# Optimization experiments

Measured on AMD Instinct MI355X. Metric: run time of the kernel, lower is better.

Reference implementation:

```python
import jax, jax.numpy as jnp
import numpy as np
from jax import lax

D_MODEL = 512
EXPAND = 2
INNER = D_MODEL * EXPAND
K = 4
B, T = 8, 2048
LN_EPS = 1e-5


def setup_inputs() -> dict:
    key = jax.random.key(0)
    ks = jax.random.split(key, 12)
    s_in = 1.0 / np.sqrt(D_MODEL)
    s_out = 1.0 / np.sqrt(INNER)
    return {
        "x": jax.random.normal(ks[0], (B, T, D_MODEL), dtype=jnp.float32),
        "ln_w": jnp.ones((D_MODEL,), jnp.float32),
        "ln_b": jnp.zeros((D_MODEL,), jnp.float32),
        "in_proj_w": jax.random.uniform(ks[1], (3 * INNER, D_MODEL), jnp.float32, -s_in, s_in),
        "in_proj_b": jax.random.uniform(ks[2], (3 * INNER,), jnp.float32, -s_in, s_in),
        "conv_w": jax.random.uniform(ks[3], (INNER, 1, K), jnp.float32, -0.5, 0.5),
        "conv_b": jax.random.uniform(ks[4], (INNER,), jnp.float32, -0.5, 0.5),
        "delta_w": jax.random.uniform(ks[5], (INNER, D_MODEL), jnp.float32, -s_in, s_in),
        "delta_b": jax.random.uniform(ks[6], (INNER,), jnp.float32, -s_in, s_in),
        "state_mix": jnp.zeros((INNER,), jnp.float32),
        "skip_scale": jnp.ones((INNER,), jnp.float32),
        "out_proj_w": jax.random.uniform(ks[7], (D_MODEL, INNER), jnp.float32, -s_out, s_out),
        "out_proj_b": jax.random.uniform(ks[8], (D_MODEL,), jnp.float32, -s_out, s_out),
    }


def _layernorm(x, w, b):
    mu = jnp.mean(x, axis=-1, keepdims=True)
    var = jnp.mean(jnp.square(x - mu), axis=-1, keepdims=True)
    return (x - mu) * lax.rsqrt(var + LN_EPS) * w + b


def _causal_dw_conv(x_bct, w, b):
    # x: [B, C, T], w: [C, 1, K] depthwise, left pad K-1 (causal)
    y = lax.conv_general_dilated(
        x_bct, w, window_strides=(1,), padding=[(K - 1, 0)],
        dimension_numbers=("NCH", "OIH", "NCH"), feature_group_count=INNER)
    return y + b[None, :, None]


def reference(x, ln_w, ln_b, in_proj_w, in_proj_b, conv_w, conv_b,
              delta_w, delta_b, state_mix, skip_scale, out_proj_w, out_proj_b):
    residual = x
    xn = _layernorm(x, ln_w, ln_b)                      # [B,T,D]
    h = xn @ in_proj_w.T + in_proj_b                     # [B,T,3*INNER]
    proj, gate, drive = jnp.split(h, 3, axis=-1)
    proj = jax.nn.silu(proj)
    gate = jax.nn.sigmoid(gate)
    conv_out = _causal_dw_conv(jnp.swapaxes(proj, 1, 2), conv_w, conv_b)
    conv_out = jnp.swapaxes(conv_out, 1, 2)              # [B,T,INNER]
    delta = jnp.maximum(jax.nn.sigmoid(xn @ delta_w.T + delta_b), 1e-4)
    drive = jnp.tanh(drive)
    a = jax.nn.sigmoid(state_mix)                        # [INNER]
    d = delta * drive                                    # [B,T,INNER]

    def step(state, d_t):
        state = a * state + d_t
        return state, state

    _, states = lax.scan(step, jnp.zeros((x.shape[0], INNER), x.dtype),
                         jnp.swapaxes(d, 0, 1))          # [T,B,INNER]
    states = jnp.swapaxes(states, 0, 1)                  # [B,T,INNER]
    y = (states + skip_scale * conv_out) * gate
    y = y @ out_proj_w.T + out_proj_b
    return residual + y
```

## Files before the change

### kernel.cpp

```cpp
#include <hip/hip_runtime.h>
#include <stdint.h>

#define D_MODEL 512
#define INNER   1024
#define NCAT    4096
#define BATCH   8
#define SEQ     2048
#define ROWS    (BATCH*SEQ)
#define LN_EPS  1e-5f
#define CHUNK   64
#define NCHUNK  (SEQ/CHUNK)

typedef unsigned short u16;
typedef unsigned int   u32;
typedef __attribute__((ext_vector_type(8))) short bf16x8;
typedef __attribute__((ext_vector_type(4))) float f32x4;

__device__ __forceinline__ u16 f2bf(float f) {
  u32 u = __builtin_bit_cast(u32, f);
  return (u16)((u + 0x7FFFu + ((u >> 16) & 1u)) >> 16);
}
__device__ __forceinline__ float bf2f(u32 lo) {
  return __builtin_bit_cast(float, lo << 16);
}
__device__ __forceinline__ float sigf(float x){ return 1.f/(1.f+__expf(-x)); }

__device__ __forceinline__ void glds16(const void* g, void* l) {
  __builtin_amdgcn_global_load_lds((const __attribute__((address_space(1))) void*)g,
                                   (__attribute__((address_space(3))) void*)l, 16, 0, 0);
}

#define MFMA16(a,b,c) __builtin_amdgcn_mfma_f32_16x16x32_bf16((a),(b),(c),0,0,0)

__global__ __launch_bounds__(256) void ln_kernel(const float* __restrict__ x,
    const float* __restrict__ lw, const float* __restrict__ lb,
    u16* __restrict__ xn) {
  const int row  = blockIdx.x * 4 + (threadIdx.x >> 6);
  const int lane = threadIdx.x & 63;
  const float4* xr = (const float4*)(x + (size_t)row * D_MODEL);
  float4 v0 = xr[lane*2], v1 = xr[lane*2+1];
  float s  = v0.x+v0.y+v0.z+v0.w + v1.x+v1.y+v1.z+v1.w;
  float s2 = v0.x*v0.x+v0.y*v0.y+v0.z*v0.z+v0.w*v0.w
           + v1.x*v1.x+v1.y*v1.y+v1.z*v1.z+v1.w*v1.w;
  #pragma unroll
  for (int o=32;o;o>>=1){ s += __shfl_xor(s,o); s2 += __shfl_xor(s2,o); }
  const float mu = s * (1.f/D_MODEL);
  const float rs = rsqrtf(s2*(1.f/D_MODEL) - mu*mu + LN_EPS);
  const float4* wv = (const float4*)lw; const float4* bv = (const float4*)lb;
  float4 w0 = wv[lane*2], w1 = wv[lane*2+1];
  float4 b0 = bv[lane*2], b1 = bv[lane*2+1];
  u32 p0 = (u32)f2bf((v0.x-mu)*rs*w0.x+b0.x) | ((u32)f2bf((v0.y-mu)*rs*w0.y+b0.y)<<16);
  u32 p1 = (u32)f2bf((v0.z-mu)*rs*w0.z+b0.z) | ((u32)f2bf((v0.w-mu)*rs*w0.w+b0.w)<<16);
  u32 p2 = (u32)f2bf((v1.x-mu)*rs*w1.x+b1.x) | ((u32)f2bf((v1.y-mu)*rs*w1.y+b1.y)<<16);
  u32 p3 = (u32)f2bf((v1.z-mu)*rs*w1.z+b1.z) | ((u32)f2bf((v1.w-mu)*rs*w1.w+b1.w)<<16);
  ((uint4*)(xn + (size_t)row * D_MODEL))[lane] = make_uint4(p0,p1,p2,p3);
}

__global__ __launch_bounds__(256) void cvt_all_kernel(const float* __restrict__ ipw,
    const float* __restrict__ dw, const float* __restrict__ opw,
    const float* __restrict__ ipb, const float* __restrict__ db,
    u16* __restrict__ wcat, u16* __restrict__ wout, float* __restrict__ bcat) {
  const int i = blockIdx.x*256 + threadIdx.x;
  const int NW1 = NCAT*D_MODEL, NW2 = D_MODEL*INNER, STR = gridDim.x*256;
  for (int idx = i; idx < NW1; idx += STR) {
    const int r = idx >> 9, c = idx & 511;
    float v;
    if (r < 2048) v = ipw[idx];
    else {
      const int rr = r - 2048;
      v = (rr & 1) ? dw[(size_t)(rr>>1)*D_MODEL + c]
                   : ipw[(size_t)(2048 + (rr>>1))*D_MODEL + c];
    }
    wcat[idx] = f2bf(v);
  }
  for (int idx = i; idx < NW2; idx += STR) wout[idx] = f2bf(opw[idx]);
  if (i < NCAT) {
    float b;
    if (i < 2048) b = ipb[i];
    else { const int rr = i - 2048; b = (rr & 1) ? db[rr>>1] : ipb[2048 + (rr>>1)]; }
    bcat[i] = b;
  }
}

__device__ __forceinline__ void sched_blk(int nbm, int nbn, int GM, int GN,
                                          int& bM, int& bN) {
  const int nwg = nbm * nbn;
  const int bid = blockIdx.x;
  const int cpx = nwg >> 3;
  const int swz = (bid & 7) * cpx + (bid >> 3);
  const int gsz = GM * GN;
  const int g   = swz / gsz, loc = swz - g * gsz;
  const int ngn = nbn / GN;
  const int gm  = g / ngn,  gn  = g - gm * ngn;
  bM = gm * GM + (loc % GM);
  bN = gn * GN + (loc / GM);
}

__device__ __forceinline__ void gemm_main(const u16* __restrict__ A,
    const u16* __restrict__ Bm, int K, int nkt, int bM, int bN,
    u16* lA, u16* lB, f32x4 acc[4][4]) {
  const int tid = threadIdx.x;
  const int l6  = tid >> 2;
  const int sg  = (tid & 3) ^ (l6 & 3);
  const int pB  = (l6 & 15) * 4 + ((l6 >> 4) & 3);
  const u16* gA = A  + (size_t)(bM*128 + l6)*K + sg*8;
  const u16* gB = Bm + (size_t)(bN*128 + pB)*K + sg*8;
  u16* dA = lA + tid*8;
  u16* dB = lB + tid*8;
  const size_t rstep = (size_t)64*K;

#define STAGE_T(koff, bufo) do { \
    const u16* sA = gA + (koff); const u16* sB = gB + (koff); \
    glds16(sA,         dA + (bufo));        glds16(sA + rstep, dA + (bufo) + 2048); \
    glds16(sB,         dB + (bufo));        glds16(sB + rstep, dB + (bufo) + 2048); \
  } while (0)

  STAGE_T(0, 0);
  STAGE_T(32, 4096);
  asm volatile("s_waitcnt vmcnt(4)" ::: "memory");
  __builtin_amdgcn_s_barrier();
  __builtin_amdgcn_sched_barrier(0);

  const int lane = tid & 63, wv = tid >> 6;
  const int wm = wv >> 1, wn = wv & 1;
  const int kx = ((lane>>4) ^ (lane&3)) * 8;
  const int aoff = (wm*64 + (lane&15))*32 + kx;
  const int boff = (wn*64 + (lane&15))*32 + kx;

  int cur = 0, stg = 8192;
  for (int kt = 0; kt < nkt; ++kt) {
    bf16x8 af[4], bfr[4];
    #pragma unroll
    for (int m=0;m<4;m++) af[m]  = *(const bf16x8*)&lA[cur + aoff + m*512];
    #pragma unroll
    for (int n=0;n<4;n++) bfr[n] = *(const bf16x8*)&lB[cur + boff + n*512];
    if (kt + 2 < nkt) STAGE_T((kt+2)*32, stg);
    #pragma unroll
    for (int m=0;m<4;m++)
      #pragma unroll
      for (int n=0;n<4;n++)
        acc[m][n] = MFMA16(af[m], bfr[n], acc[m][n]);
    if (kt + 2 < nkt) { asm volatile("s_waitcnt vmcnt(4)" ::: "memory"); }
    else              { asm volatile("s_waitcnt vmcnt(0)" ::: "memory"); }
    __builtin_amdgcn_s_barrier();
    __builtin_amdgcn_sched_barrier(0);
    cur += 4096; if (cur == 12288) cur = 0;
    stg += 4096; if (stg == 12288) stg = 0;
  }
#undef STAGE_T
}

__global__ __launch_bounds__(256, 3) void gemm1_kernel(const u16* __restrict__ A,
    const u16* __restrict__ Bm, const float* __restrict__ bcat,
    u16* __restrict__ proj, u16* __restrict__ gate, u16* __restrict__ dbuf) {
  __shared__ u16 lA[12288], lB[12288];
  f32x4 acc[4][4];
  #pragma unroll
  for (int m=0;m<4;m++)
    #pragma unroll
    for (int n=0;n<4;n++) acc[m][n] = (f32x4){0.f,0.f,0.f,0.f};
  int bM, bN; sched_blk(ROWS/128, NCAT/128, 16, 8, bM, bN);
  gemm_main(A, Bm, D_MODEL, D_MODEL/32, bM, bN, lA, lB, acc);
  const int lane = threadIdx.x & 63, wv = threadIdx.x >> 6;
  const int wm = wv>>1, wn = wv&1;
  const int colb = bN*128 + wn*64 + (lane&15)*4;
  const float4 b4 = *(const float4*)&bcat[colb];
  const float* bp = (const float*)&b4;
  if (colb < 2048) {
    u16* outp = (colb < 1024) ? proj : gate;
    const int lcolb = colb & (INNER-1);
    #pragma unroll
    for (int m=0;m<4;m++) {
      const int row0 = bM*128 + wm*64 + m*16 + ((lane>>4)<<2);
      #pragma unroll
      for (int r=0;r<4;r++) {
        float a4[4];
        #pragma unroll
        for (int n=0;n<4;n++) {
          float v = acc[m][n][r] + bp[n];
          a4[n] = (colb < 1024) ? v * sigf(v) : sigf(v);
        }
        u32 lo = (u32)f2bf(a4[0]) | ((u32)f2bf(a4[1])<<16);
        u32 hi = (u32)f2bf(a4[2]) | ((u32)f2bf(a4[3])<<16);
        *(uint2*)&outp[(size_t)(row0+r)*INNER + lcolb] = make_uint2(lo, hi);
      }
    }
  } else {
    const int ch0 = (colb - 2048) >> 1;
    #pragma unroll
    for (int m=0;m<4;m++) {
      const int row0 = bM*128 + wm*64 + m*16 + ((lane>>4)<<2);
      #pragma unroll
      for (int r=0;r<4;r++) {
        const float v0 = acc[m][0][r] + bp[0];
        const float v1 = acc[m][1][r] + bp[1];
        const float v2 = acc[m][2][r] + bp[2];
        const float v3 = acc[m][3][r] + bp[3];
        const float d0 = (2.f*sigf(2.f*v0) - 1.f) * fmaxf(sigf(v1), 1e-4f);
        const float d1 = (2.f*sigf(2.f*v2) - 1.f) * fmaxf(sigf(v3), 1e-4f);
        *(u32*)&dbuf[(size_t)(row0+r)*INNER + ch0] = (u32)f2bf(d0) | ((u32)f2bf(d1)<<16);
      }
    }
  }
}

__global__ __launch_bounds__(256, 3) void gemm2_kernel(const u16* __restrict__ A,
    const u16* __restrict__ Bm, const float* __restrict__ ob,
    const float* __restrict__ resid, float* __restrict__ out) {
  __shared__ u16 lA[12288], lB[12288];
  f32x4 acc[4][4];
  #pragma unroll
  for (int m=0;m<4;m++)
    #pragma unroll
    for (int n=0;n<4;n++) acc[m][n] = (f32x4){0.f,0.f,0.f,0.f};
  int bM, bN; sched_blk(ROWS/128, D_MODEL/128, 8, 4, bM, bN);
  gemm_main(A, Bm, INNER, INNER/32, bM, bN, lA, lB, acc);
  const int lane = threadIdx.x & 63, wv = threadIdx.x >> 6;
  const int wm = wv>>1, wn = wv&1;
  const int colb = bN*128 + wn*64 + (lane&15)*4;
  const float4 ob4 = *(const float4*)&ob[colb];
  #pragma unroll
  for (int m=0;m<4;m++) {
    const int row0 = bM*128 + wm*64 + m*16 + ((lane>>4)<<2);
    #pragma unroll
    for (int r=0;r<4;r++) {
      const size_t idx = (size_t)(row0+r)*D_MODEL + colb;
      float4 rs = *(const float4*)&resid[idx];
      float4 o;
      o.x = acc[m][0][r] + ob4.x + rs.x;
      o.y = acc[m][1][r] + ob4.y + rs.y;
      o.z = acc[m][2][r] + ob4.z + rs.z;
      o.w = acc[m][3][r] + ob4.w + rs.w;
      *(float4*)&out[idx] = o;
    }
  }
}

__global__ __launch_bounds__(256) void scan1_kernel(const u16* __restrict__ d,
    const float* __restrict__ sm, float* __restrict__ cS) {
  const int blk = blockIdx.x;
  const int half = blk & 1, ch = (blk>>1) & (NCHUNK-1), b = blk >> 6;
  const int c0 = half*512 + threadIdx.x*2;
  const float a0 = sigf(sm[c0]), a1 = sigf(sm[c0+1]);
  float s0 = 0.f, s1 = 0.f;
  size_t base = ((size_t)b*SEQ + ch*CHUNK)*INNER + c0;
  for (int t=0;t<CHUNK;t++) {
    u32 du = *(const u32*)(d + base);
    s0 = a0*s0 + bf2f(du & 0xffffu);
    s1 = a1*s1 + bf2f(du >> 16);
    base += INNER;
  }
  const size_t o = ((size_t)b*NCHUNK + ch)*INNER + c0;
  cS[o] = s0; cS[o+1] = s1;
}

__global__ __launch_bounds__(256) void scan2_kernel(const float* __restrict__ sm,
    const float* __restrict__ cS, float* __restrict__ carry) {
  const int idx = blockIdx.x*256 + threadIdx.x;
  const int b = idx >> 9, c0 = (idx & 511)*2;
  const float a0 = sigf(sm[c0]), a1 = sigf(sm[c0+1]);
  float A0 = a0, A1 = a1;
  #pragma unroll
  for (int i=0;i<6;i++){ A0*=A0; A1*=A1; }
  float cr0 = 0.f, cr1 = 0.f;
  for (int ch=0; ch<NCHUNK; ch++) {
    const size_t o = ((size_t)b*NCHUNK + ch)*INNER + c0;
    carry[o] = cr0; carry[o+1] = cr1;
    cr0 = A0*cr0 + cS[o];
    cr1 = A1*cr1 + cS[o+1];
  }
}

__global__ __launch_bounds__(256) void scan3_kernel(const u16* __restrict__ proj,
    const u16* __restrict__ gate, const u16* __restrict__ d,
    const float* __restrict__ carry, const float* __restrict__ sm,
    const float* __restrict__ cw, const float* __restrict__ cb,
    const float* __restrict__ sk, u16* __restrict__ z) {
  const int blk = blockIdx.x;
  const int half = blk & 1, ch = (blk>>1) & (NCHUNK-1), b = blk >> 6;
  const int c0 = half*512 + threadIdx.x*2;
  const float a0 = sigf(sm[c0]), a1 = sigf(sm[c0+1]);
  const float cb0 = cb[c0], cb1 = cb[c0+1];
  const float sk0 = sk[c0], sk1 = sk[c0+1];
  const float w00=cw[c0*4+0], w01=cw[c0*4+1], w02=cw[c0*4+2], w03=cw[c0*4+3];
  const float w10=cw[c0*4+4], w11=cw[c0*4+5], w12=cw[c0*4+6], w13=cw[c0*4+7];
  const size_t o = ((size_t)b*NCHUNK + ch)*INNER + c0;
  float s0 = carry[o], s1 = carry[o+1];
  const int t0 = ch*CHUNK;
  const size_t rowb = (size_t)b*SEQ*INNER + c0;
  float pa0=0,pb0=0,pc0=0, pa1=0,pb1=0,pc1=0;
  if (ch > 0) {
    u32 u3 = *(const u32*)(proj + rowb + (size_t)(t0-3)*INNER);
    u32 u2 = *(const u32*)(proj + rowb + (size_t)(t0-2)*INNER);
    u32 u1 = *(const u32*)(proj + rowb + (size_t)(t0-1)*INNER);
    pa0 = bf2f(u3&0xffffu); pa1 = bf2f(u3>>16);
    pb0 = bf2f(u2&0xffffu); pb1 = bf2f(u2>>16);
    pc0 = bf2f(u1&0xffffu); pc1 = bf2f(u1>>16);
  }
  size_t base = rowb + (size_t)t0*INNER;
  for (int t=0;t<CHUNK;t++) {
    u32 pu = *(const u32*)(proj + base);
    const float pd0 = bf2f(pu&0xffffu), pd1 = bf2f(pu>>16);
    const float co0 = w00*pa0 + w01*pb0 + w02*pc0 + w03*pd0 + cb0;
    const float co1 = w10*pa1 + w11*pb1 + w12*pc1 + w13*pd1 + cb1;
    pa0=pb0; pb0=pc0; pc0=pd0;  pa1=pb1; pb1=pc1; pc1=pd1;
    u32 du = *(const u32*)(d + base);
    s0 = a0*s0 + bf2f(du&0xffffu);
    s1 = a1*s1 + bf2f(du>>16);
    u32 gu = *(const u32*)(gate + base);
    const float z0 = (s0 + sk0*co0)*bf2f(gu&0xffffu);
    const float z1 = (s1 + sk1*co1)*bf2f(gu>>16);
    *(u32*)(z + base) = (u32)f2bf(z0) | ((u32)f2bf(z1)<<16);
    base += INNER;
  }
}

extern "C" void kernel_launch(void* const* d_in, const int* in_sizes, int n_in,
                              void* d_out, int out_size, void* d_ws, size_t ws_size,
                              hipStream_t stream) {
  const float* x    = (const float*)d_in[0];
  const float* ln_w = (const float*)d_in[1];
  const float* ln_b = (const float*)d_in[2];
  const float* ipw  = (const float*)d_in[3];
  const float* ipb  = (const float*)d_in[4];
  const float* cw   = (const float*)d_in[5];
  const float* cb   = (const float*)d_in[6];
  const float* dw   = (const float*)d_in[7];
  const float* db   = (const float*)d_in[8];
  const float* sm   = (const float*)d_in[9];
  const float* sk   = (const float*)d_in[10];
  const float* opw  = (const float*)d_in[11];
  const float* opb  = (const float*)d_in[12];
  float* out = (float*)d_out;

  uint8_t* w = (uint8_t*)d_ws;
  u16* xn    = (u16*)w;  w += (size_t)ROWS*D_MODEL*2;
  u16* wcat  = (u16*)w;  w += (size_t)NCAT*D_MODEL*2;
  u16* wout  = (u16*)w;  w += (size_t)D_MODEL*INNER*2;
  u16* proj  = (u16*)w;  w += (size_t)ROWS*INNER*2;
  u16* gate  = (u16*)w;  w += (size_t)ROWS*INNER*2;
  u16* dbuf  = (u16*)w;  w += (size_t)ROWS*INNER*2;
  u16* z     = (u16*)w;  w += (size_t)ROWS*INNER*2;
  float* cS    = (float*)w; w += (size_t)BATCH*NCHUNK*INNER*4;
  float* carry = (float*)w; w += (size_t)BATCH*NCHUNK*INNER*4;
  float* bcat  = (float*)w; w += (size_t)NCAT*4;

  ln_kernel<<<ROWS/4, 256, 0, stream>>>(x, ln_w, ln_b, xn);
  cvt_all_kernel<<<1024, 256, 0, stream>>>(ipw, dw, opw, ipb, db, wcat, wout, bcat);
  gemm1_kernel<<<(ROWS/128)*(NCAT/128), 256, 0, stream>>>(xn, wcat, bcat, proj, gate, dbuf);
  scan1_kernel<<<BATCH*NCHUNK*2, 256, 0, stream>>>(dbuf, sm, cS);
  scan2_kernel<<<16, 256, 0, stream>>>(sm, cS, carry);
  scan3_kernel<<<BATCH*NCHUNK*2, 256, 0, stream>>>(proj, gate, dbuf, carry, sm, cw, cb, sk, z);
  gemm2_kernel<<<(ROWS/128)*(D_MODEL/128), 256, 0, stream>>>(z, wout, opb, x, out);
}
```

Measured before the change: 168.1 us.

## Enlarge gemm1 to 256x256 tiles with 512 threads and dynamic LDS

Rewrites the first projection GEMM as a standalone kernel using 256x256 output tiles, 8 waves each computing 128x64, with a new swizzled LDS layout held in 96KB of dynamic shared memory across three stages. The larger tile raises arithmetic intensity and cuts global and LDS traffic per FLOP for the dominant GEMM. In exchange, occupancy drops to at most 2 blocks per CU, register pressure rises with 32 accumulators per thread, and the grid shrinks to 1024 blocks, which may leave wave-quantisation tail effects.

```diff
diff --git a/kernel.cpp b/kernel.cpp
--- a/kernel.cpp
+++ b/kernel.cpp
@@ -96,82 +96,83 @@
   bN = gn * GN + (loc / GM);
 }
 
-__device__ __forceinline__ void gemm_main(const u16* __restrict__ A,
-    const u16* __restrict__ Bm, int K, int nkt, int bM, int bN,
-    u16* lA, u16* lB, f32x4 acc[4][4]) {
+__global__ __launch_bounds__(512, 2) void gemm1_kernel(const u16* __restrict__ A,
+    const u16* __restrict__ Bm, const float* __restrict__ bcat,
+    u16* __restrict__ proj, u16* __restrict__ gate, u16* __restrict__ dbuf) {
+  extern __shared__ u16 lds[];
   const int tid = threadIdx.x;
-  const int l6  = tid >> 2;
-  const int sg  = (tid & 3) ^ (l6 & 3);
-  const int pB  = (l6 & 15) * 4 + ((l6 >> 4) & 3);
-  const u16* gA = A  + (size_t)(bM*128 + l6)*K + sg*8;
-  const u16* gB = Bm + (size_t)(bN*128 + pB)*K + sg*8;
-  u16* dA = lA + tid*8;
-  u16* dB = lB + tid*8;
-  const size_t rstep = (size_t)64*K;
-
-#define STAGE_T(koff, bufo) do { \
-    const u16* sA = gA + (koff); const u16* sB = gB + (koff); \
-    glds16(sA,         dA + (bufo));        glds16(sA + rstep, dA + (bufo) + 2048); \
-    glds16(sB,         dB + (bufo));        glds16(sB + rstep, dB + (bufo) + 2048); \
-  } while (0)
-
-  STAGE_T(0, 0);
-  STAGE_T(32, 4096);
+  int bM, bN; sched_blk(ROWS/256, NCAT/256, 8, 4, bM, bN);
+
+  const u16* gA0; const u16* gA1; const u16* gB0; const u16* gB1;
+  {
+    const int p0 = tid,        q0 = p0>>3, t0 = (p0&7) ^ (q0&7);
+    const int p1 = 512 + tid,  q1 = p1>>3, t1 = (p1&7) ^ (q1&7);
+    const int rA0 = q0*2 + (t0>>2), sA0 = t0&3;
+    const int rA1 = q1*2 + (t1>>2), sA1 = t1&3;
+    gA0 = A + (size_t)(bM*256 + rA0)*D_MODEL + sA0*8;
+    gA1 = A + (size_t)(bM*256 + rA1)*D_MODEL + sA1*8;
+    const int c0 = (rA0 & ~63) + ((rA0&15)*4) + ((rA0>>4)&3);
+    const int c1 = (rA1 & ~63) + ((rA1&15)*4) + ((rA1>>4)&3);
+    gB0 = Bm + (size_t)(bN*256 + c0)*D_MODEL + sA0*8;
+    gB1 = Bm + (size_t)(bN*256 + c1)*D_MODEL + sA1*8;
+  }
+
+#define STAGE1(KOFF, BUFO) do { \
+    glds16(gA0 + (KOFF), lds + (BUFO) + tid*8); \
+    glds16(gA1 + (KOFF), lds + (BUFO) + 4096 + tid*8); \
+    glds16(gB0 + (KOFF), lds + (BUFO) + 8192 + tid*8); \
+    glds16(gB1 + (KOFF), lds + (BUFO) + 12288 + tid*8); } while(0)
+
+  const int lane = tid & 63, wid = tid >> 6;
+  const int wm = wid >> 2, wn = wid & 3;
+  const int rl = lane & 15;
+  const int e  = (((lane&1)<<2) + (lane>>4)) ^ (rl>>1);
+  const int aoff = wm*4096 + (rl>>1)*64 + e*8;
+  const int boff = 8192 + wn*2048 + (rl>>1)*64 + e*8;
+
+  f32x4 acc[8][4];
+  #pragma unroll
+  for (int m=0;m<8;m++)
+    #pragma unroll
+    for (int n=0;n<4;n++) acc[m][n] = (f32x4){0.f,0.f,0.f,0.f};
+
+  STAGE1(0, 0);
+  STAGE1(32, 16384);
   asm volatile("s_waitcnt vmcnt(4)" ::: "memory");
   __builtin_amdgcn_s_barrier();
   __builtin_amdgcn_sched_barrier(0);
 
-  const int lane = tid & 63, wv = tid >> 6;
-  const int wm = wv >> 1, wn = wv & 1;
-  const int kx = ((lane>>4) ^ (lane&3)) * 8;
-  const int aoff = (wm*64 + (lane&15))*32 + kx;
-  const int boff = (wn*64 + (lane&15))*32 + kx;
-
-  int cur = 0, stg = 8192;
-  for (int kt = 0; kt < nkt; ++kt) {
-    bf16x8 af[4], bfr[4];
-    #pragma unroll
-    for (int m=0;m<4;m++) af[m]  = *(const bf16x8*)&lA[cur + aoff + m*512];
-    #pragma unroll
-    for (int n=0;n<4;n++) bfr[n] = *(const bf16x8*)&lB[cur + boff + n*512];
-    if (kt + 2 < nkt) STAGE_T((kt+2)*32, stg);
-    #pragma unroll
-    for (int m=0;m<4;m++)
+  int cur = 0, stg = 32768;
+  for (int kt = 0; kt < 16; ++kt) {
+    bf16x8 af[8], bfr[4];
+    #pragma unroll
+    for (int m=0;m<8;m++) af[m]  = *(const bf16x8*)&lds[cur + aoff + m*512];
+    #pragma unroll
+    for (int n=0;n<4;n++) bfr[n] = *(const bf16x8*)&lds[cur + boff + n*512];
+    if (kt + 2 < 16) STAGE1((kt+2)*32, stg);
+    #pragma unroll
+    for (int m=0;m<8;m++)
       #pragma unroll
       for (int n=0;n<4;n++)
         acc[m][n] = MFMA16(af[m], bfr[n], acc[m][n]);
-    if (kt + 2 < nkt) { asm volatile("s_waitcnt vmcnt(4)" ::: "memory"); }
-    else              { asm volatile("s_waitcnt vmcnt(0)" ::: "memory"); }
+    if (kt + 2 < 16) { asm volatile("s_waitcnt vmcnt(4)" ::: "memory"); }
+    else             { asm volatile("s_waitcnt vmcnt(0)" ::: "memory"); }
     __builtin_amdgcn_s_barrier();
     __builtin_amdgcn_sched_barrier(0);
-    cur += 4096; if (cur == 12288) cur = 0;
-    stg += 4096; if (stg == 12288) stg = 0;
-  }
-#undef STAGE_T
-}
-
-__global__ __launch_bounds__(256, 3) void gemm1_kernel(const u16* __restrict__ A,
-    const u16* __restrict__ Bm, const float* __restrict__ bcat,
-    u16* __restrict__ proj, u16* __restrict__ gate, u16* __restrict__ dbuf) {
-  __shared__ u16 lA[12288], lB[12288];
-  f32x4 acc[4][4];
-  #pragma unroll
-  for (int m=0;m<4;m++)
-    #pragma unroll
-    for (int n=0;n<4;n++) acc[m][n] = (f32x4){0.f,0.f,0.f,0.f};
-  int bM, bN; sched_blk(ROWS/128, NCAT/128, 16, 8, bM, bN);
-  gemm_main(A, Bm, D_MODEL, D_MODEL/32, bM, bN, lA, lB, acc);
-  const int lane = threadIdx.x & 63, wv = threadIdx.x >> 6;
-  const int wm = wv>>1, wn = wv&1;
-  const int colb = bN*128 + wn*64 + (lane&15)*4;
+    cur += 16384; if (cur == 49152) cur = 0;
+    stg += 16384; if (stg == 49152) stg = 0;
+  }
+#undef STAGE1
+
+  const int colb = bN*256 + wn*64 + rl*4;
   const float4 b4 = *(const float4*)&bcat[colb];
   const float* bp = (const float*)&b4;
   if (colb < 2048) {
     u16* outp = (colb < 1024) ? proj : gate;
     const int lcolb = colb & (INNER-1);
     #pragma unroll
-    for (int m=0;m<4;m++) {
-      const int row0 = bM*128 + wm*64 + m*16 + ((lane>>4)<<2);
+    for (int m=0;m<8;m++) {
+      const int row0 = bM*256 + wm*128 + m*16 + ((lane>>4)<<2);
       #pragma unroll
       for (int r=0;r<4;r++) {
         float a4[4];
@@ -188,8 +189,8 @@
   } else {
     const int ch0 = (colb - 2048) >> 1;
     #pragma unroll
-    for (int m=0;m<4;m++) {
-      const int row0 = bM*128 + wm*64 + m*16 + ((lane>>4)<<2);
+    for (int m=0;m<8;m++) {
+      const int row0 = bM*256 + wm*128 + m*16 + ((lane>>4)<<2);
       #pragma unroll
       for (int r=0;r<4;r++) {
         const float v0 = acc[m][0][r] + bp[0];
@@ -202,6 +203,60 @@
       }
     }
   }
+}
+
+__device__ __forceinline__ void gemm_main(const u16* __restrict__ A,
+    const u16* __restrict__ Bm, int K, int nkt, int bM, int bN,
+    u16* lA, u16* lB, f32x4 acc[4][4]) {
+  const int tid = threadIdx.x;
+  const int l6  = tid >> 2;
+  const int sg  = (tid & 3) ^ (l6 & 3);
+  const int pB  = (l6 & 15) * 4 + ((l6 >> 4) & 3);
+  const u16* gA = A  + (size_t)(bM*128 + l6)*K + sg*8;
+  const u16* gB = Bm + (size_t)(bN*128 + pB)*K + sg*8;
+  u16* dA = lA + tid*8;
+  u16* dB = lB + tid*8;
+  const size_t rstep = (size_t)64*K;
+
+#define STAGE_T(koff, bufo) do { \
+    const u16* sA = gA + (koff); const u16* sB = gB + (koff); \
+    glds16(sA,         dA + (bufo));        glds16(sA + rstep, dA + (bufo) + 2048); \
+    glds16(sB,         dB + (bufo));        glds16(sB + rstep, dB + (bufo) + 2048); \
+  } while (0)
+
+  STAGE_T(0, 0);
+  STAGE_T(32, 4096);
+  asm volatile("s_waitcnt vmcnt(4)" ::: "memory");
+  __builtin_amdgcn_s_barrier();
+  __builtin_amdgcn_sched_barrier(0);
+
+  const int lane = tid & 63, wv = tid >> 6;
+  const int wm = wv >> 1, wn = wv & 1;
+  const int kx = ((lane>>4) ^ (lane&3)) * 8;
+  const int aoff = (wm*64 + (lane&15))*32 + kx;
+  const int boff = (wn*64 + (lane&15))*32 + kx;
+
+  int cur = 0, stg = 8192;
+  for (int kt = 0; kt < nkt; ++kt) {
+    bf16x8 af[4], bfr[4];
+    #pragma unroll
+    for (int m=0;m<4;m++) af[m]  = *(const bf16x8*)&lA[cur + aoff + m*512];
+    #pragma unroll
+    for (int n=0;n<4;n++) bfr[n] = *(const bf16x8*)&lB[cur + boff + n*512];
+    if (kt + 2 < nkt) STAGE_T((kt+2)*32, stg);
+    #pragma unroll
+    for (int m=0;m<4;m++)
+      #pragma unroll
+      for (int n=0;n<4;n++)
+        acc[m][n] = MFMA16(af[m], bfr[n], acc[m][n]);
+    if (kt + 2 < nkt) { asm volatile("s_waitcnt vmcnt(4)" ::: "memory"); }
+    else              { asm volatile("s_waitcnt vmcnt(0)" ::: "memory"); }
+    __builtin_amdgcn_s_barrier();
+    __builtin_amdgcn_sched_barrier(0);
+    cur += 4096; if (cur == 12288) cur = 0;
+    stg += 4096; if (stg == 12288) stg = 0;
+  }
+#undef STAGE_T
 }
 
 __global__ __launch_bounds__(256, 3) void gemm2_kernel(const u16* __restrict__ A,
@@ -347,7 +402,7 @@
 
   ln_kernel<<<ROWS/4, 256, 0, stream>>>(x, ln_w, ln_b, xn);
   cvt_all_kernel<<<1024, 256, 0, stream>>>(ipw, dw, opw, ipb, db, wcat, wout, bcat);
-  gemm1_kernel<<<(ROWS/128)*(NCAT/128), 256, 0, stream>>>(xn, wcat, bcat, proj, gate, dbuf);
+  gemm1_kernel<<<(ROWS/256)*(NCAT/256), 512, 98304, stream>>>(xn, wcat, bcat, proj, gate, dbuf);
   scan1_kernel<<<BATCH*NCHUNK*2, 256, 0, stream>>>(dbuf, sm, cS);
   scan2_kernel<<<16, 256, 0, stream>>>(sm, cS, carry);
   scan3_kernel<<<BATCH*NCHUNK*2, 256, 0, stream>>>(proj, gate, dbuf, carry, sm, cw, cb, sk, z);
```

New measurement: 173.8 us. 3.4% more time.

## Rewrite gemm1 as 256x256 tile, 8-wave ping-pong pipelined kernel

Applied to the files above, without the earlier changes.

Replaces the 128x128 tile, 4-wave gemm1 with a 256x256 tile, 512-thread kernel that uses 128KB of dynamic LDS with K=64 double buffering. Loads are split into half-tiles interleaved with four MFMA phases, and s_setprio plus barriers coordinate waves. The larger tile raises arithmetic intensity and cuts global traffic. The phased schedule tries to overlap global-to-LDS copies with MFMA work. In exchange, occupancy drops and register pressure rises, since each wave holds 32 accumulators, and the launch needs 128KB of shared memory per block.

```diff
diff --git a/kernel.cpp b/kernel.cpp
--- a/kernel.cpp
+++ b/kernel.cpp
@@ -96,82 +96,127 @@
   bN = gn * GN + (loc / GM);
 }
 
-__device__ __forceinline__ void gemm_main(const u16* __restrict__ A,
-    const u16* __restrict__ Bm, int K, int nkt, int bM, int bN,
-    u16* lA, u16* lB, f32x4 acc[4][4]) {
+__global__ __launch_bounds__(512, 2) void gemm1_kernel(const u16* __restrict__ A,
+    const u16* __restrict__ Bm, const float* __restrict__ bcat,
+    u16* __restrict__ proj, u16* __restrict__ gate, u16* __restrict__ dbuf) {
+  extern __shared__ u16 lds[];
   const int tid = threadIdx.x;
-  const int l6  = tid >> 2;
-  const int sg  = (tid & 3) ^ (l6 & 3);
-  const int pB  = (l6 & 15) * 4 + ((l6 >> 4) & 3);
-  const u16* gA = A  + (size_t)(bM*128 + l6)*K + sg*8;
-  const u16* gB = Bm + (size_t)(bN*128 + pB)*K + sg*8;
-  u16* dA = lA + tid*8;
-  u16* dB = lB + tid*8;
-  const size_t rstep = (size_t)64*K;
-
-#define STAGE_T(koff, bufo) do { \
-    const u16* sA = gA + (koff); const u16* sB = gB + (koff); \
-    glds16(sA,         dA + (bufo));        glds16(sA + rstep, dA + (bufo) + 2048); \
-    glds16(sB,         dB + (bufo));        glds16(sB + rstep, dB + (bufo) + 2048); \
-  } while (0)
-
-  STAGE_T(0, 0);
-  STAGE_T(32, 4096);
+  int bM, bN; sched_blk(ROWS/256, NCAT/256, 8, 4, bM, bN);
+
+  const int rS = tid >> 3;
+  const int cS = (tid & 7) ^ (rS & 7);
+  const u16* gAb = A  + (size_t)(bM*256 + rS)*D_MODEL + cS*8;
+  const u16* gBb = Bm + (size_t)(bN*256 + (rS&15)*4 + ((rS>>4)&3))*D_MODEL + cS*8;
+
+#define SA(h, kt, slot) do { \
+    glds16(gAb + (size_t)(h)*65536 + (kt)*64,         lds + (slot) + (h)*8192 + tid*8); \
+    glds16(gAb + (size_t)(h)*65536 + 32768 + (kt)*64, lds + (slot) + (h)*8192 + 4096 + tid*8); } while(0)
+#define SB(h, kt, slot) do { \
+    glds16(gBb + (size_t)(h)*65536 + (kt)*64,         lds + (slot) + 16384 + (h)*8192 + tid*8); \
+    glds16(gBb + (size_t)(h)*65536 + 32768 + (kt)*64, lds + (slot) + 16384 + (h)*8192 + 4096 + tid*8); } while(0)
+
+  const int lane = tid & 63, wid = tid >> 6;
+  const int wm = wid >> 2, wn = wid & 3;
+  const int ksw = ((lane>>4) ^ (lane&7)) * 8;
+  const int aW = wm*8192 + (lane&15)*64 + ksw;
+  const int bW = 16384 + wn*4096 + (lane&15)*64 + ksw;
+
+  f32x4 acc[8][4];
+  #pragma unroll
+  for (int m=0;m<8;m++)
+    #pragma unroll
+    for (int n=0;n<4;n++) acc[m][n] = (f32x4){0.f,0.f,0.f,0.f};
+  bf16x8 af[4][2], bf0[2][2], bf1[2][2];
+
+#define RD_A(mh, s) do { _Pragma("unroll") \
+    for (int mm=0; mm<4; ++mm) { \
+      af[mm][0] = *(const bf16x8*)&lds[(s) + aW + (mh)*4096 + mm*1024]; \
+      af[mm][1] = *(const bf16x8*)&lds[((s) + aW + (mh)*4096 + mm*1024) ^ 32]; \
+    } } while(0)
+#define RD_B0(s) do { \
+    bf0[0][0] = *(const bf16x8*)&lds[(s) + bW];            bf0[0][1] = *(const bf16x8*)&lds[((s) + bW) ^ 32]; \
+    bf0[1][0] = *(const bf16x8*)&lds[(s) + bW + 1024];     bf0[1][1] = *(const bf16x8*)&lds[((s) + bW + 1024) ^ 32]; } while(0)
+#define RD_B1(s) do { \
+    bf1[0][0] = *(const bf16x8*)&lds[(s) + bW + 2048];     bf1[0][1] = *(const bf16x8*)&lds[((s) + bW + 2048) ^ 32]; \
+    bf1[1][0] = *(const bf16x8*)&lds[(s) + bW + 3072];     bf1[1][1] = *(const bf16x8*)&lds[((s) + bW + 3072) ^ 32]; } while(0)
+#define PH_SYNC do { \
+    __builtin_amdgcn_s_barrier(); \
+    asm volatile("s_waitcnt lgkmcnt(0)" ::: "memory"); \
+    __builtin_amdgcn_sched_barrier(0); \
+    __builtin_amdgcn_s_setprio(1); } while(0)
+#define PH_END do { \
+    __builtin_amdgcn_s_setprio(0); \
+    __builtin_amdgcn_s_barrier(); } while(0)
+#define MM_Q(ML, NL, BF) do { _Pragma("unroll") \
+    for (int mm=0; mm<4; ++mm) { \
+      acc[(ML)+mm][(NL)  ] = MFMA16(af[mm][0], BF[0][0], acc[(ML)+mm][(NL)  ]); \
+      acc[(ML)+mm][(NL)  ] = MFMA16(af[mm][1], BF[0][1], acc[(ML)+mm][(NL)  ]); \
+      acc[(ML)+mm][(NL)+1] = MFMA16(af[mm][0], BF[1][0], acc[(ML)+mm][(NL)+1]); \
+      acc[(ML)+mm][(NL)+1] = MFMA16(af[mm][1], BF[1][1], acc[(ML)+mm][(NL)+1]); \
+    } } while(0)
+
+  SA(0,0,0); SA(1,0,0); SB(0,0,0); SB(1,0,0);
+  SB(0,1,32768); SB(1,1,32768);
   asm volatile("s_waitcnt vmcnt(4)" ::: "memory");
   __builtin_amdgcn_s_barrier();
-  __builtin_amdgcn_sched_barrier(0);
-
-  const int lane = tid & 63, wv = tid >> 6;
-  const int wm = wv >> 1, wn = wv & 1;
-  const int kx = ((lane>>4) ^ (lane&3)) * 8;
-  const int aoff = (wm*64 + (lane&15))*32 + kx;
-  const int boff = (wn*64 + (lane&15))*32 + kx;
-
-  int cur = 0, stg = 8192;
-  for (int kt = 0; kt < nkt; ++kt) {
-    bf16x8 af[4], bfr[4];
-    #pragma unroll
-    for (int m=0;m<4;m++) af[m]  = *(const bf16x8*)&lA[cur + aoff + m*512];
-    #pragma unroll
-    for (int n=0;n<4;n++) bfr[n] = *(const bf16x8*)&lB[cur + boff + n*512];
-    if (kt + 2 < nkt) STAGE_T((kt+2)*32, stg);
-    #pragma unroll
-    for (int m=0;m<4;m++)
-      #pragma unroll
-      for (int n=0;n<4;n++)
-        acc[m][n] = MFMA16(af[m], bfr[n], acc[m][n]);
-    if (kt + 2 < nkt) { asm volatile("s_waitcnt vmcnt(4)" ::: "memory"); }
-    else              { asm volatile("s_waitcnt vmcnt(0)" ::: "memory"); }
+
+  #pragma unroll
+  for (int i = 0; i < 4; ++i) {
+    const int e = 2*i, o = e+1;
+    RD_A(0, 0); RD_B0(0);
+    SA(0, o, 32768);
+    PH_SYNC; MM_Q(0,0,bf0); PH_END;
+    RD_B1(0);
+    SA(1, o, 32768);
+    PH_SYNC; MM_Q(0,2,bf1); PH_END;
+    RD_A(1, 0);
+    if (i < 3) SB(0, e+2, 0);
+    PH_SYNC; MM_Q(4,2,bf1); PH_END;
+    if (i < 3) SB(1, e+2, 0);
     __builtin_amdgcn_s_barrier();
-    __builtin_amdgcn_sched_barrier(0);
-    cur += 4096; if (cur == 12288) cur = 0;
-    stg += 4096; if (stg == 12288) stg = 0;
-  }
-#undef STAGE_T
-}
-
-__global__ __launch_bounds__(256, 3) void gemm1_kernel(const u16* __restrict__ A,
-    const u16* __restrict__ Bm, const float* __restrict__ bcat,
-    u16* __restrict__ proj, u16* __restrict__ gate, u16* __restrict__ dbuf) {
-  __shared__ u16 lA[12288], lB[12288];
-  f32x4 acc[4][4];
-  #pragma unroll
-  for (int m=0;m<4;m++)
-    #pragma unroll
-    for (int n=0;n<4;n++) acc[m][n] = (f32x4){0.f,0.f,0.f,0.f};
-  int bM, bN; sched_blk(ROWS/128, NCAT/128, 16, 8, bM, bN);
-  gemm_main(A, Bm, D_MODEL, D_MODEL/32, bM, bN, lA, lB, acc);
-  const int lane = threadIdx.x & 63, wv = threadIdx.x >> 6;
-  const int wm = wv>>1, wn = wv&1;
-  const int colb = bN*128 + wn*64 + (lane&15)*4;
+    __builtin_amdgcn_s_setprio(1);
+    MM_Q(4,0,bf0);
+    __builtin_amdgcn_s_setprio(0);
+    if (i < 3) { asm volatile("s_waitcnt vmcnt(4)" ::: "memory"); }
+    else       { asm volatile("s_waitcnt vmcnt(0)" ::: "memory"); }
+    __builtin_amdgcn_s_barrier();
+    RD_A(0, 32768); RD_B0(32768);
+    if (i < 3) SA(0, e+2, 0);
+    PH_SYNC; MM_Q(0,0,bf0); PH_END;
+    RD_B1(32768);
+    if (i < 3) SA(1, e+2, 0);
+    PH_SYNC; MM_Q(0,2,bf1); PH_END;
+    RD_A(1, 32768);
+    if (i < 3) SB(0, o+2, 32768);
+    PH_SYNC; MM_Q(4,2,bf1); PH_END;
+    if (i < 3) SB(1, o+2, 32768);
+    __builtin_amdgcn_s_barrier();
+    __builtin_amdgcn_s_setprio(1);
+    MM_Q(4,0,bf0);
+    __builtin_amdgcn_s_setprio(0);
+    if (i < 3) { asm volatile("s_waitcnt vmcnt(4)" ::: "memory"); }
+    else       { asm volatile("s_waitcnt vmcnt(0)" ::: "memory"); }
+    __builtin_amdgcn_s_barrier();
+  }
+#undef SA
+#undef SB
+#undef RD_A
+#undef RD_B0
+#undef RD_B1
+#undef PH_SYNC
+#undef PH_END
+#undef MM_Q
+
+  const int rl = lane & 15;
+  const int colb = bN*256 + wn*64 + rl*4;
   const float4 b4 = *(const float4*)&bcat[colb];
   const float* bp = (const float*)&b4;
   if (colb < 2048) {
     u16* outp = (colb < 1024) ? proj : gate;
     const int lcolb = colb & (INNER-1);
     #pragma unroll
-    for (int m=0;m<4;m++) {
-      const int row0 = bM*128 + wm*64 + m*16 + ((lane>>4)<<2);
+    for (int m=0;m<8;m++) {
+      const int row0 = bM*256 + wm*128 + m*16 + ((lane>>4)<<2);
       #pragma unroll
       for (int r=0;r<4;r++) {
         float a4[4];
@@ -188,8 +233,8 @@
   } else {
     const int ch0 = (colb - 2048) >> 1;
     #pragma unroll
-    for (int m=0;m<4;m++) {
-      const int row0 = bM*128 + wm*64 + m*16 + ((lane>>4)<<2);
+    for (int m=0;m<8;m++) {
+      const int row0 = bM*256 + wm*128 + m*16 + ((lane>>4)<<2);
       #pragma unroll
       for (int r=0;r<4;r++) {
         const float v0 = acc[m][0][r] + bp[0];
@@ -202,6 +247,60 @@
       }
     }
   }
+}
+
+__device__ __forceinline__ void gemm_main(const u16* __restrict__ A,
+    const u16* __restrict__ Bm, int K, int nkt, int bM, int bN,
+    u16* lA, u16* lB, f32x4 acc[4][4]) {
+  const int tid = threadIdx.x;
+  const int l6  = tid >> 2;
+  const int sg  = (tid & 3) ^ (l6 & 3);
+  const int pB  = (l6 & 15) * 4 + ((l6 >> 4) & 3);
+  const u16* gA = A  + (size_t)(bM*128 + l6)*K + sg*8;
+  const u16* gB = Bm + (size_t)(bN*128 + pB)*K + sg*8;
+  u16* dA = lA + tid*8;
+  u16* dB = lB + tid*8;
+  const size_t rstep = (size_t)64*K;
+
+#define STAGE_T(koff, bufo) do { \
+    const u16* sA = gA + (koff); const u16* sB = gB + (koff); \
+    glds16(sA,         dA + (bufo));        glds16(sA + rstep, dA + (bufo) + 2048); \
+    glds16(sB,         dB + (bufo));        glds16(sB + rstep, dB + (bufo) + 2048); \
+  } while (0)
+
+  STAGE_T(0, 0);
+  STAGE_T(32, 4096);
+  asm volatile("s_waitcnt vmcnt(4)" ::: "memory");
+  __builtin_amdgcn_s_barrier();
+  __builtin_amdgcn_sched_barrier(0);
+
+  const int lane = tid & 63, wv = tid >> 6;
+  const int wm = wv >> 1, wn = wv & 1;
+  const int kx = ((lane>>4) ^ (lane&3)) * 8;
+  const int aoff = (wm*64 + (lane&15))*32 + kx;
+  const int boff = (wn*64 + (lane&15))*32 + kx;
+
+  int cur = 0, stg = 8192;
+  for (int kt = 0; kt < nkt; ++kt) {
+    bf16x8 af[4], bfr[4];
+    #pragma unroll
+    for (int m=0;m<4;m++) af[m]  = *(const bf16x8*)&lA[cur + aoff + m*512];
+    #pragma unroll
+    for (int n=0;n<4;n++) bfr[n] = *(const bf16x8*)&lB[cur + boff + n*512];
+    if (kt + 2 < nkt) STAGE_T((kt+2)*32, stg);
+    #pragma unroll
+    for (int m=0;m<4;m++)
+      #pragma unroll
+      for (int n=0;n<4;n++)
+        acc[m][n] = MFMA16(af[m], bfr[n], acc[m][n]);
+    if (kt + 2 < nkt) { asm volatile("s_waitcnt vmcnt(4)" ::: "memory"); }
+    else              { asm volatile("s_waitcnt vmcnt(0)" ::: "memory"); }
+    __builtin_amdgcn_s_barrier();
+    __builtin_amdgcn_sched_barrier(0);
+    cur += 4096; if (cur == 12288) cur = 0;
+    stg += 4096; if (stg == 12288) stg = 0;
+  }
+#undef STAGE_T
 }
 
 __global__ __launch_bounds__(256, 3) void gemm2_kernel(const u16* __restrict__ A,
@@ -347,7 +446,7 @@
 
   ln_kernel<<<ROWS/4, 256, 0, stream>>>(x, ln_w, ln_b, xn);
   cvt_all_kernel<<<1024, 256, 0, stream>>>(ipw, dw, opw, ipb, db, wcat, wout, bcat);
-  gemm1_kernel<<<(ROWS/128)*(NCAT/128), 256, 0, stream>>>(xn, wcat, bcat, proj, gate, dbuf);
+  gemm1_kernel<<<(ROWS/256)*(NCAT/256), 512, 131072, stream>>>(xn, wcat, bcat, proj, gate, dbuf);
   scan1_kernel<<<BATCH*NCHUNK*2, 256, 0, stream>>>(dbuf, sm, cS);
   scan2_kernel<<<16, 256, 0, stream>>>(sm, cS, carry);
   scan3_kernel<<<BATCH*NCHUNK*2, 256, 0, stream>>>(proj, gate, dbuf, carry, sm, cw, cb, sk, z);
```

After: 169.9 us. No clear change (+1.1%).
